# Kernel optimization log

Measured on AMD Instinct MI355X. Metric: run time of the kernel, lower is better.

Reference implementation:

```python
import jax, jax.numpy as jnp
import numpy as np

B, T, I, H = 4096, 120, 64, 128


def setup_inputs() -> dict:
    key = jax.random.key(0)
    ks = jax.random.split(key, 5)
    s = 1.0 / np.sqrt(H)
    return {
        "x": jax.random.normal(ks[0], (B, T, I), dtype=jnp.float32),
        "W_ih": jax.random.uniform(ks[1], (3 * H, I), jnp.float32, -s, s),
        "W_hh": jax.random.uniform(ks[2], (3 * H, H), jnp.float32, -s, s),
        "b_ih": jax.random.uniform(ks[3], (3 * H,), jnp.float32, -s, s),
        "b_hh": jax.random.uniform(ks[4], (3 * H,), jnp.float32, -s, s),
    }


def reference(x, W_ih, W_hh, b_ih, b_hh):
    # x: [B, T, I]; PyTorch GRUCell gate order: reset, update, new.
    Bv, Tv, _ = x.shape
    Hv = W_hh.shape[1]
    # Precompute input-side gate projections for all timesteps (same math,
    # hoisted out of the recurrence): [B, T, 3H]
    x_gates = jnp.einsum("bti,gi->btg", x, W_ih) + b_ih

    def step(h, xg_t):
        hg = h @ W_hh.T + b_hh  # [B, 3H]
        xr, xz, xn = jnp.split(xg_t, 3, axis=-1)
        hr, hz, hn = jnp.split(hg, 3, axis=-1)
        r = jax.nn.sigmoid(xr + hr)
        z = jax.nn.sigmoid(xz + hz)
        n = jnp.tanh(xn + r * hn)
        h_new = (1.0 - z) * n + z * h
        return h_new, h_new

    h0 = jnp.zeros((Bv, Hv), dtype=x.dtype)
    h_T, outs = jax.lax.scan(step, h0, jnp.swapaxes(x_gates, 0, 1))  # outs: [T, B, H]
    outputs = jnp.swapaxes(outs, 0, 1)  # [B, T, H]
    return outputs, h_T
```

## Files before the change

### kernel.cpp

```cpp
#include <hip/hip_runtime.h>
#include <hip/hip_bf16.h>


#define Bv 4096
#define Tv 120
#define Iv 64
#define Hv 128

typedef __attribute__((ext_vector_type(8))) short short8;
typedef __attribute__((ext_vector_type(4))) float floatx4;

#if __has_builtin(__builtin_amdgcn_exp2f)
#define EXP2F(x) __builtin_amdgcn_exp2f(x)
#else
#define EXP2F(x) exp2f(x)
#endif
#if __has_builtin(__builtin_amdgcn_rcpf)
#define RCPF(x) __builtin_amdgcn_rcpf(x)
#else
#define RCPF(x) (1.0f / (x))
#endif

__device__ inline short f2bf(float f) {
    union { float f; unsigned u; } v; v.f = f;
    unsigned r = v.u + 0x7FFFu + ((v.u >> 16) & 1u);
    return (short)(r >> 16);
}

__device__ inline float sigmoid_fast(float x) {
    return RCPF(1.0f + EXP2F(-1.44269504f * x));
}
__device__ inline float tanh_fast(float x) {
    return 1.0f - 2.0f * RCPF(1.0f + EXP2F(2.88539008f * x));
}

__launch_bounds__(512, 2)
__global__ void gru_persist(const float* __restrict__ x,
                            const float* __restrict__ W_ih,
                            const float* __restrict__ W_hh,
                            const float* __restrict__ b_ih,
                            const float* __restrict__ b_hh,
                            float* __restrict__ out) {
    constexpr int XSTR = 72;
    constexpr int HSTR = 136;
    __shared__ short h_lds[16 * HSTR];
    __shared__ short x_lds[2][16 * XSTR];

    const int tid  = threadIdx.x;
    const int wave = tid >> 6;
    const int lane = tid & 63;
    const int s    = lane & 15;
    const int quad = lane >> 4;
    const int b0   = blockIdx.x * 16;
    const int c    = wave * 16 + s;

    const float bias_r  = b_ih[c] + b_hh[c];
    const float bias_z  = b_ih[c + 128] + b_hh[c + 128];
    const float bias_xn = b_ih[c + 256];
    const float bias_hn = b_hh[c + 256];

    short8 whh[3][4];
    short8 wih[3][2];
#pragma unroll
    for (int g = 0; g < 3; ++g) {
        const float* wr = W_hh + (size_t)(g * 128 + c) * 128;
#pragma unroll
        for (int kst = 0; kst < 4; ++kst) {
            const float* p = wr + kst * 32 + quad * 8;
            floatx4 lo = *(const floatx4*)p;
            floatx4 hi = *(const floatx4*)(p + 4);
            short8 f;
            f[0] = f2bf(lo[0]); f[1] = f2bf(lo[1]); f[2] = f2bf(lo[2]); f[3] = f2bf(lo[3]);
            f[4] = f2bf(hi[0]); f[5] = f2bf(hi[1]); f[6] = f2bf(hi[2]); f[7] = f2bf(hi[3]);
            whh[g][kst] = f;
        }
        const float* wi = W_ih + (size_t)(g * 128 + c) * 64;
#pragma unroll
        for (int kst = 0; kst < 2; ++kst) {
            const float* p = wi + kst * 32 + quad * 8;
            floatx4 lo = *(const floatx4*)p;
            floatx4 hi = *(const floatx4*)(p + 4);
            short8 f;
            f[0] = f2bf(lo[0]); f[1] = f2bf(lo[1]); f[2] = f2bf(lo[2]); f[3] = f2bf(lo[3]);
            f[4] = f2bf(hi[0]); f[5] = f2bf(hi[1]); f[6] = f2bf(hi[2]); f[7] = f2bf(hi[3]);
            wih[g][kst] = f;
        }
    }

    for (int i = tid; i < 16 * HSTR; i += 512) h_lds[i] = 0;
    float hcar[4] = {0.f, 0.f, 0.f, 0.f};

    const int xrow = tid >> 5, xcp = tid & 31;
    const float* xbase = x + ((size_t)(b0 + xrow) * Tv) * Iv + xcp * 2;
    {
        float2 v = *(const float2*)xbase;
        unsigned pk = (unsigned short)f2bf(v.x) | ((unsigned)(unsigned short)f2bf(v.y) << 16);
        *(unsigned*)&x_lds[0][xrow * XSTR + xcp * 2] = pk;
    }
    __syncthreads();

    float* hT = out + (size_t)Bv * Tv * Hv;
    const size_t obase = ((size_t)(b0 + quad * 4) * Tv) * Hv + c;

#pragma unroll 1
    for (int t = 0; t < Tv; ++t) {
        float2 xv;
        if (t + 1 < Tv) xv = *(const float2*)(xbase + (size_t)(t + 1) * Iv);

        const short* hrow = &h_lds[s * HSTR];
        short8 ah0 = *(const short8*)(hrow + quad * 8);
        short8 ah1 = *(const short8*)(hrow + 32 + quad * 8);
        short8 ah2 = *(const short8*)(hrow + 64 + quad * 8);
        short8 ah3 = *(const short8*)(hrow + 96 + quad * 8);
        const short* xr = &x_lds[t & 1][s * XSTR];
        short8 ax0 = *(const short8*)(xr + quad * 8);
        short8 ax1 = *(const short8*)(xr + 32 + quad * 8);

        floatx4 accr  = {bias_r, bias_r, bias_r, bias_r};
        floatx4 accz  = {bias_z, bias_z, bias_z, bias_z};
        floatx4 accxn = {bias_xn, bias_xn, bias_xn, bias_xn};
        floatx4 acchn = {bias_hn, bias_hn, bias_hn, bias_hn};

        accr  = __builtin_amdgcn_mfma_f32_16x16x32_bf16(ah0, whh[0][0], accr, 0, 0, 0);
        accz  = __builtin_amdgcn_mfma_f32_16x16x32_bf16(ah0, whh[1][0], accz, 0, 0, 0);
        acchn = __builtin_amdgcn_mfma_f32_16x16x32_bf16(ah0, whh[2][0], acchn, 0, 0, 0);
        accr  = __builtin_amdgcn_mfma_f32_16x16x32_bf16(ah1, whh[0][1], accr, 0, 0, 0);
        accz  = __builtin_amdgcn_mfma_f32_16x16x32_bf16(ah1, whh[1][1], accz, 0, 0, 0);
        acchn = __builtin_amdgcn_mfma_f32_16x16x32_bf16(ah1, whh[2][1], acchn, 0, 0, 0);
        accr  = __builtin_amdgcn_mfma_f32_16x16x32_bf16(ah2, whh[0][2], accr, 0, 0, 0);
        accz  = __builtin_amdgcn_mfma_f32_16x16x32_bf16(ah2, whh[1][2], accz, 0, 0, 0);
        acchn = __builtin_amdgcn_mfma_f32_16x16x32_bf16(ah2, whh[2][2], acchn, 0, 0, 0);
        accr  = __builtin_amdgcn_mfma_f32_16x16x32_bf16(ah3, whh[0][3], accr, 0, 0, 0);
        accz  = __builtin_amdgcn_mfma_f32_16x16x32_bf16(ah3, whh[1][3], accz, 0, 0, 0);
        acchn = __builtin_amdgcn_mfma_f32_16x16x32_bf16(ah3, whh[2][3], acchn, 0, 0, 0);

        accr  = __builtin_amdgcn_mfma_f32_16x16x32_bf16(ax0, wih[0][0], accr, 0, 0, 0);
        accz  = __builtin_amdgcn_mfma_f32_16x16x32_bf16(ax0, wih[1][0], accz, 0, 0, 0);
        accxn = __builtin_amdgcn_mfma_f32_16x16x32_bf16(ax0, wih[2][0], accxn, 0, 0, 0);
        accr  = __builtin_amdgcn_mfma_f32_16x16x32_bf16(ax1, wih[0][1], accr, 0, 0, 0);
        accz  = __builtin_amdgcn_mfma_f32_16x16x32_bf16(ax1, wih[1][1], accz, 0, 0, 0);
        accxn = __builtin_amdgcn_mfma_f32_16x16x32_bf16(ax1, wih[2][1], accxn, 0, 0, 0);

        __syncthreads();

#pragma unroll
        for (int r = 0; r < 4; ++r) {
            float rg = sigmoid_fast(accr[r]);
            float zg = sigmoid_fast(accz[r]);
            float ng = tanh_fast(accxn[r] + rg * acchn[r]);
            float h  = (1.0f - zg) * ng + zg * hcar[r];
            hcar[r] = h;
            out[obase + (size_t)r * Tv * Hv + (size_t)t * Hv] = h;
            h_lds[(quad * 4 + r) * HSTR + c] = f2bf(h);
            if (t == Tv - 1) hT[(size_t)(b0 + quad * 4 + r) * Hv + c] = h;
        }

        if (t + 1 < Tv) {
            unsigned pk = (unsigned short)f2bf(xv.x) | ((unsigned)(unsigned short)f2bf(xv.y) << 16);
            *(unsigned*)&x_lds[(t + 1) & 1][xrow * XSTR + xcp * 2] = pk;
        }
        __syncthreads();
    }
}

extern "C" void kernel_launch(void* const* d_in, const int* in_sizes, int n_in,
                              void* d_out, int out_size, void* d_ws, size_t ws_size,
                              hipStream_t stream) {
    (void)in_sizes; (void)n_in; (void)out_size; (void)d_ws; (void)ws_size;
    const float* x    = (const float*)d_in[0];
    const float* W_ih = (const float*)d_in[1];
    const float* W_hh = (const float*)d_in[2];
    const float* b_ih = (const float*)d_in[3];
    const float* b_hh = (const float*)d_in[4];
    float* out = (float*)d_out;
    hipLaunchKernelGGL(gru_persist, dim3(Bv / 16), dim3(512), 0, stream,
                       x, W_ih, W_hh, b_ih, b_hh, out);
}
```

Measured before the change: 418.0 us.

## Double-buffer hidden state in LDS, transpose MFMA operands for vectorized stores

The hidden-state LDS buffer is double-buffered, which removes one of the two barriers per timestep; the remaining barrier is a raw s_barrier after an lgkmcnt wait. MFMA operands are swapped so each lane holds four consecutive hidden columns for one batch row. This allows float4 output stores, packed bf16 writes via v_cvt_pk_bf16_f32, vector bias loads, and a single final h_T store outside the loop. The loop is also unrolled by 2 and the gate math uses FMAs, at the cost of extra LDS space and reliance on inline asm.

```diff
diff --git a/kernel.cpp b/kernel.cpp
--- a/kernel.cpp
+++ b/kernel.cpp
@@ -1,5 +1,4 @@
 #include <hip/hip_runtime.h>
-#include <hip/hip_bf16.h>
 
 
 #define Bv 4096
@@ -9,6 +8,7 @@
 
 typedef __attribute__((ext_vector_type(8))) short short8;
 typedef __attribute__((ext_vector_type(4))) float floatx4;
+typedef __attribute__((ext_vector_type(2))) unsigned uintx2;
 
 #if __has_builtin(__builtin_amdgcn_exp2f)
 #define EXP2F(x) __builtin_amdgcn_exp2f(x)
@@ -27,6 +27,12 @@
     return (short)(r >> 16);
 }
 
+__device__ inline unsigned cvt_pk_bf16(float a, float b) {
+    unsigned d;
+    asm("v_cvt_pk_bf16_f32 %0, %1, %2" : "=v"(d) : "v"(a), "v"(b));
+    return d;
+}
+
 __device__ inline float sigmoid_fast(float x) {
     return RCPF(1.0f + EXP2F(-1.44269504f * x));
 }
@@ -43,7 +49,7 @@
                             float* __restrict__ out) {
     constexpr int XSTR = 72;
     constexpr int HSTR = 136;
-    __shared__ short h_lds[16 * HSTR];
+    __shared__ short h_lds[2][16 * HSTR];
     __shared__ short x_lds[2][16 * XSTR];
 
     const int tid  = threadIdx.x;
@@ -53,11 +59,12 @@
     const int quad = lane >> 4;
     const int b0   = blockIdx.x * 16;
     const int c    = wave * 16 + s;
+    const int cb   = wave * 16 + quad * 4;
 
-    const float bias_r  = b_ih[c] + b_hh[c];
-    const float bias_z  = b_ih[c + 128] + b_hh[c + 128];
-    const float bias_xn = b_ih[c + 256];
-    const float bias_hn = b_hh[c + 256];
+    floatx4 bias_r  = *(const floatx4*)(b_ih + cb)       + *(const floatx4*)(b_hh + cb);
+    floatx4 bias_z  = *(const floatx4*)(b_ih + 128 + cb) + *(const floatx4*)(b_hh + 128 + cb);
+    floatx4 bias_xn = *(const floatx4*)(b_ih + 256 + cb);
+    floatx4 bias_hn = *(const floatx4*)(b_hh + 256 + cb);
 
     short8 whh[3][4];
     short8 wih[3][2];
@@ -87,80 +94,82 @@
         }
     }
 
-    for (int i = tid; i < 16 * HSTR; i += 512) h_lds[i] = 0;
-    float hcar[4] = {0.f, 0.f, 0.f, 0.f};
+    for (int i = tid; i < 16 * HSTR; i += 512) h_lds[0][i] = 0;
+    floatx4 hcar = {0.f, 0.f, 0.f, 0.f};
 
     const int xrow = tid >> 5, xcp = tid & 31;
     const float* xbase = x + ((size_t)(b0 + xrow) * Tv) * Iv + xcp * 2;
     {
         float2 v = *(const float2*)xbase;
-        unsigned pk = (unsigned short)f2bf(v.x) | ((unsigned)(unsigned short)f2bf(v.y) << 16);
-        *(unsigned*)&x_lds[0][xrow * XSTR + xcp * 2] = pk;
+        *(unsigned*)&x_lds[0][xrow * XSTR + xcp * 2] = cvt_pk_bf16(v.x, v.y);
     }
     __syncthreads();
 
-    float* hT = out + (size_t)Bv * Tv * Hv;
-    const size_t obase = ((size_t)(b0 + quad * 4) * Tv) * Hv + c;
+    float* optr = out + ((size_t)(b0 + s) * Tv) * Hv + cb;
+    float* hT   = out + (size_t)Bv * Tv * Hv;
 
-#pragma unroll 1
+#pragma unroll 2
     for (int t = 0; t < Tv; ++t) {
-        float2 xv;
-        if (t + 1 < Tv) xv = *(const float2*)(xbase + (size_t)(t + 1) * Iv);
+        const int hb = t & 1;
+        const int tn = (t + 1 < Tv) ? (t + 1) : t;
+        float2 xv = *(const float2*)(xbase + (size_t)tn * Iv);
 
-        const short* hrow = &h_lds[s * HSTR];
+        const short* hrow = &h_lds[hb][s * HSTR];
         short8 ah0 = *(const short8*)(hrow + quad * 8);
         short8 ah1 = *(const short8*)(hrow + 32 + quad * 8);
         short8 ah2 = *(const short8*)(hrow + 64 + quad * 8);
         short8 ah3 = *(const short8*)(hrow + 96 + quad * 8);
-        const short* xr = &x_lds[t & 1][s * XSTR];
+        const short* xr = &x_lds[hb][s * XSTR];
         short8 ax0 = *(const short8*)(xr + quad * 8);
         short8 ax1 = *(const short8*)(xr + 32 + quad * 8);
 
-        floatx4 accr  = {bias_r, bias_r, bias_r, bias_r};
-        floatx4 accz  = {bias_z, bias_z, bias_z, bias_z};
-        floatx4 accxn = {bias_xn, bias_xn, bias_xn, bias_xn};
-        floatx4 acchn = {bias_hn, bias_hn, bias_hn, bias_hn};
+        floatx4 accr  = __builtin_amdgcn_mfma_f32_16x16x32_bf16(whh[0][0], ah0, bias_r, 0, 0, 0);
+        floatx4 accz  = __builtin_amdgcn_mfma_f32_16x16x32_bf16(whh[1][0], ah0, bias_z, 0, 0, 0);
+        floatx4 acchn = __builtin_amdgcn_mfma_f32_16x16x32_bf16(whh[2][0], ah0, bias_hn, 0, 0, 0);
+        accr  = __builtin_amdgcn_mfma_f32_16x16x32_bf16(whh[0][1], ah1, accr, 0, 0, 0);
+        accz  = __builtin_amdgcn_mfma_f32_16x16x32_bf16(whh[1][1], ah1, accz, 0, 0, 0);
+        acchn = __builtin_amdgcn_mfma_f32_16x16x32_bf16(whh[2][1], ah1, acchn, 0, 0, 0);
+        accr  = __builtin_amdgcn_mfma_f32_16x16x32_bf16(whh[0][2], ah2, accr, 0, 0, 0);
+        accz  = __builtin_amdgcn_mfma_f32_16x16x32_bf16(whh[1][2], ah2, accz, 0, 0, 0);
+        acchn = __builtin_amdgcn_mfma_f32_16x16x32_bf16(whh[2][2], ah2, acchn, 0, 0, 0);
+        accr  = __builtin_amdgcn_mfma_f32_16x16x32_bf16(whh[0][3], ah3, accr, 0, 0, 0);
+        accz  = __builtin_amdgcn_mfma_f32_16x16x32_bf16(whh[1][3], ah3, accz, 0, 0, 0);
+        acchn = __builtin_amdgcn_mfma_f32_16x16x32_bf16(whh[2][3], ah3, acchn, 0, 0, 0);
 
-        accr  = __builtin_amdgcn_mfma_f32_16x16x32_bf16(ah0, whh[0][0], accr, 0, 0, 0);
-        accz  = __builtin_amdgcn_mfma_f32_16x16x32_bf16(ah0, whh[1][0], accz, 0, 0, 0);
-        acchn = __builtin_amdgcn_mfma_f32_16x16x32_bf16(ah0, whh[2][0], acchn, 0, 0, 0);
-        accr  = __builtin_amdgcn_mfma_f32_16x16x32_bf16(ah1, whh[0][1], accr, 0, 0, 0);
-        accz  = __builtin_amdgcn_mfma_f32_16x16x32_bf16(ah1, whh[1][1], accz, 0, 0, 0);
-        acchn = __builtin_amdgcn_mfma_f32_16x16x32_bf16(ah1, whh[2][1], acchn, 0, 0, 0);
-        accr  = __builtin_amdgcn_mfma_f32_16x16x32_bf16(ah2, whh[0][2], accr, 0, 0, 0);
-        accz  = __builtin_amdgcn_mfma_f32_16x16x32_bf16(ah2, whh[1][2], accz, 0, 0, 0);
-        acchn = __builtin_amdgcn_mfma_f32_16x16x32_bf16(ah2, whh[2][2], acchn, 0, 0, 0);
-        accr  = __builtin_amdgcn_mfma_f32_16x16x32_bf16(ah3, whh[0][3], accr, 0, 0, 0);
-        accz  = __builtin_amdgcn_mfma_f32_16x16x32_bf16(ah3, whh[1][3], accz, 0, 0, 0);
-        acchn = __builtin_amdgcn_mfma_f32_16x16x32_bf16(ah3, whh[2][3], acchn, 0, 0, 0);
+        floatx4 accxn = __builtin_amdgcn_mfma_f32_16x16x32_bf16(wih[2][0], ax0, bias_xn, 0, 0, 0);
+        accr  = __builtin_amdgcn_mfma_f32_16x16x32_bf16(wih[0][0], ax0, accr, 0, 0, 0);
+        accz  = __builtin_amdgcn_mfma_f32_16x16x32_bf16(wih[1][0], ax0, accz, 0, 0, 0);
+        accxn = __builtin_amdgcn_mfma_f32_16x16x32_bf16(wih[2][1], ax1, accxn, 0, 0, 0);
+        accr  = __builtin_amdgcn_mfma_f32_16x16x32_bf16(wih[0][1], ax1, accr, 0, 0, 0);
+        accz  = __builtin_amdgcn_mfma_f32_16x16x32_bf16(wih[1][1], ax1, accz, 0, 0, 0);
 
-        accr  = __builtin_amdgcn_mfma_f32_16x16x32_bf16(ax0, wih[0][0], accr, 0, 0, 0);
-        accz  = __builtin_amdgcn_mfma_f32_16x16x32_bf16(ax0, wih[1][0], accz, 0, 0, 0);
-        accxn = __builtin_amdgcn_mfma_f32_16x16x32_bf16(ax0, wih[2][0], accxn, 0, 0, 0);
-        accr  = __builtin_amdgcn_mfma_f32_16x16x32_bf16(ax1, wih[0][1], accr, 0, 0, 0);
-        accz  = __builtin_amdgcn_mfma_f32_16x16x32_bf16(ax1, wih[1][1], accz, 0, 0, 0);
-        accxn = __builtin_amdgcn_mfma_f32_16x16x32_bf16(ax1, wih[2][1], accxn, 0, 0, 0);
-
-        __syncthreads();
-
+        floatx4 hv;
 #pragma unroll
         for (int r = 0; r < 4; ++r) {
             float rg = sigmoid_fast(accr[r]);
             float zg = sigmoid_fast(accz[r]);
-            float ng = tanh_fast(accxn[r] + rg * acchn[r]);
-            float h  = (1.0f - zg) * ng + zg * hcar[r];
+            float ng = tanh_fast(fmaf(rg, acchn[r], accxn[r]));
+            float h  = fmaf(zg, hcar[r] - ng, ng);
             hcar[r] = h;
-            out[obase + (size_t)r * Tv * Hv + (size_t)t * Hv] = h;
-            h_lds[(quad * 4 + r) * HSTR + c] = f2bf(h);
-            if (t == Tv - 1) hT[(size_t)(b0 + quad * 4 + r) * Hv + c] = h;
+            hv[r]   = h;
         }
 
-        if (t + 1 < Tv) {
-            unsigned pk = (unsigned short)f2bf(xv.x) | ((unsigned)(unsigned short)f2bf(xv.y) << 16);
-            *(unsigned*)&x_lds[(t + 1) & 1][xrow * XSTR + xcp * 2] = pk;
-        }
-        __syncthreads();
+        *(unsigned*)&x_lds[hb ^ 1][xrow * XSTR + xcp * 2] = cvt_pk_bf16(xv.x, xv.y);
+
+        uintx2 hp;
+        hp[0] = cvt_pk_bf16(hv[0], hv[1]);
+        hp[1] = cvt_pk_bf16(hv[2], hv[3]);
+        *(uintx2*)&h_lds[hb ^ 1][s * HSTR + cb] = hp;
+
+        *(floatx4*)optr = hv;
+        optr += Hv;
+
+        asm volatile("s_waitcnt lgkmcnt(0)" ::: "memory");
+        __builtin_amdgcn_s_barrier();
+        asm volatile("" ::: "memory");
     }
+
+    *(floatx4*)(hT + (size_t)(b0 + s) * Hv + cb) = hcar;
 }
 
 extern "C" void kernel_launch(void* const* d_in, const int* in_sizes, int n_in,
```

After: 432.9 us. 3.6% more time.
